# Kernel optimization log

Measured on AMD Instinct MI355X. Metric: run time of the kernel, lower is better.

The kernel has to match this reference:

```python
import jax, jax.numpy as jnp
import numpy as np

B, T, C, H, DH = 4, 2048, 1024, 16, 64  # batch, seq (block_size), n_embd, heads, head_size


def setup_inputs() -> dict:
    key = jax.random.key(0)
    ks = jax.random.split(key, 6)
    x = jax.random.normal(ks[0], (B, T, C), dtype=jnp.float32)
    init = 0.02
    Wq = jax.random.normal(ks[1], (H, C, DH), dtype=jnp.float32) * init
    Wk = jax.random.normal(ks[2], (H, C, DH), dtype=jnp.float32) * init
    Wv = jax.random.normal(ks[3], (H, C, DH), dtype=jnp.float32) * init
    Wp = jax.random.normal(ks[4], (H * DH, C), dtype=jnp.float32) * init
    bp = jnp.zeros((C,), dtype=jnp.float32)
    return {"x": x, "Wq": Wq, "Wk": Wk, "Wv": Wv, "Wp": Wp, "bp": bp}


def reference(x, Wq, Wk, Wv, Wp, bp):
    Bb, Tt, Cc = x.shape
    # per-head projections, vectorized over heads (original loops in Python)
    q = jnp.einsum('btc,hcd->bhtd', x, Wq)
    k = jnp.einsum('btc,hcd->bhtd', x, Wk)
    v = jnp.einsum('btc,hcd->bhtd', x, Wv)
    # NOTE: original scales by rsqrt(C) where C is the INPUT embed dim, not head_size
    scale = 1.0 / jnp.sqrt(jnp.asarray(Cc, dtype=x.dtype))
    wei = jnp.einsum('bhtd,bhsd->bhts', q, k) * scale  # [B,H,T,T]
    causal = jnp.tril(jnp.ones((Tt, Tt), dtype=bool))
    wei = jnp.where(causal, wei, -jnp.inf)
    wei = jax.nn.softmax(wei, axis=-1)
    out = jnp.einsum('bhts,bhsd->bhtd', wei, v)  # [B,H,T,DH]
    # concat heads along feature axis (head h -> slice h*DH:(h+1)*DH)
    out = out.transpose(0, 2, 1, 3).reshape(Bb, Tt, -1)  # [B,T,H*DH]
    out = out @ Wp + bp  # output projection to n_embd
    return out
```

## Files before the change

kernel.cpp:

```cpp
#include <hip/hip_runtime.h>

#define TSEQ 2048
#define CDIM 1024
#define NH 16
#define DH 64
#define NB 4

typedef __bf16 bf16x8 __attribute__((ext_vector_type(8)));
typedef float f32x4 __attribute__((ext_vector_type(4)));

#define QSCALE 0.04508422f

static __device__ __forceinline__ ushort f2bf(float f) {
  unsigned u = __float_as_uint(f);
  unsigned r = u + 0x7fffu + ((u >> 16) & 1u);
  return (ushort)(r >> 16);
}

static __device__ __forceinline__ void gload_lds16(const void* g, void* ldsbase) {
  __builtin_amdgcn_global_load_lds((const __attribute__((address_space(1))) void*)g,
                                   (__attribute__((address_space(3))) void*)ldsbase,
                                   16, 0, 0);
}

__global__ void cvt_x_kernel(const float4* __restrict__ src, ushort4* __restrict__ dst, int n4) {
  int i = blockIdx.x * blockDim.x + threadIdx.x;
  if (i >= n4) return;
  float4 f = src[i];
  ushort4 o;
  o.x = f2bf(f.x); o.y = f2bf(f.y); o.z = f2bf(f.z); o.w = f2bf(f.w);
  dst[i] = o;
}

__global__ void transpose_cvt_kernel(const float* __restrict__ src, ushort* __restrict__ dst,
                                     int R, int Cc) {
  __shared__ float tile[32][33];
  const float* s = src + (size_t)blockIdx.z * R * Cc;
  ushort* d = dst + (size_t)blockIdx.z * R * Cc;
  int c0 = blockIdx.x * 32, r0 = blockIdx.y * 32;
  int tx = threadIdx.x, ty = threadIdx.y;
  for (int i = ty; i < 32; i += 8) {
    int r = r0 + i, c = c0 + tx;
    tile[i][tx] = (r < R && c < Cc) ? s[(size_t)r * Cc + c] : 0.f;
  }
  __syncthreads();
  for (int i = ty; i < 32; i += 8) {
    int c = c0 + i, r = r0 + tx;
    if (c < Cc && r < R) d[(size_t)c * R + r] = f2bf(tile[tx][i]);
  }
}

__global__ __launch_bounds__(256) void qkv_kernel(
    const ushort* __restrict__ xb, const ushort* __restrict__ wqT,
    const ushort* __restrict__ wkT, const ushort* __restrict__ wvT,
    ushort* __restrict__ qb, ushort* __restrict__ kb, ushort* __restrict__ vTb) {
  __shared__ ushort lds[12288];
  const int tt = blockIdx.x, bh = blockIdx.y, sel = blockIdx.z;
  const int h = bh & (NH - 1);
  const int tid = threadIdx.x, w = tid >> 6, l = tid & 63;
  const ushort* A = xb + ((size_t)(bh >> 4) * TSEQ + (size_t)tt * 128) * CDIM;
  const ushort* Bw = (sel == 0 ? wqT : sel == 1 ? wkT : wvT) + (size_t)h * DH * CDIM;
  const int srow = l >> 3;
  const int scol = (((l & 7) ^ srow) << 3);
  char* ldsb = (char*)lds;

  f32x4 acc[2][4] = {};

  for (int k0 = 0; k0 < CDIM; k0 += 64) {
#pragma unroll
    for (int i = 0; i < 6; ++i) {
      int ch = w * 6 + i;
      if (ch < 16) {
        int row = ch * 8 + srow;
        gload_lds16(A + (size_t)row * CDIM + k0 + scol, ldsb + ch * 1024);
      } else {
        int row = (ch - 16) * 8 + srow;
        gload_lds16(Bw + (size_t)row * CDIM + k0 + scol, ldsb + 16384 + (ch - 16) * 1024);
      }
    }
    __syncthreads();
#pragma unroll
    for (int ks = 0; ks < 2; ++ks) {
      bf16x8 af[2];
#pragma unroll
      for (int fm = 0; fm < 2; ++fm) {
        int row = w * 32 + fm * 16 + (l & 15);
        int cb = (ks * 64 + 16 * (l >> 4)) ^ ((row & 7) << 4);
        af[fm] = *(const bf16x8*)(ldsb + row * 128 + cb);
      }
#pragma unroll
      for (int fn = 0; fn < 4; ++fn) {
        int n = fn * 16 + (l & 15);
        int cb = (ks * 64 + 16 * (l >> 4)) ^ ((n & 7) << 4);
        bf16x8 bfr = *(const bf16x8*)(ldsb + 16384 + n * 128 + cb);
#pragma unroll
        for (int fm = 0; fm < 2; ++fm)
          acc[fm][fn] = __builtin_amdgcn_mfma_f32_16x16x32_bf16(af[fm], bfr, acc[fm][fn], 0, 0, 0);
      }
    }
    __syncthreads();
  }

  const int tbase0 = tt * 128 + w * 32;
#pragma unroll
  for (int fm = 0; fm < 2; ++fm) {
#pragma unroll
    for (int fn = 0; fn < 4; ++fn) {
      int d = fn * 16 + (l & 15);
      int tb = tbase0 + fm * 16 + (l >> 4) * 4;
      if (sel == 2) {
        ushort4 pk;
        pk.x = f2bf(acc[fm][fn][0]); pk.y = f2bf(acc[fm][fn][1]);
        pk.z = f2bf(acc[fm][fn][2]); pk.w = f2bf(acc[fm][fn][3]);
        *(ushort4*)(vTb + ((size_t)bh * DH + d) * TSEQ + tb) = pk;
      } else if (sel == 0) {
#pragma unroll
        for (int r = 0; r < 4; ++r)
          qb[((size_t)bh * TSEQ + tb + r) * DH + d] = f2bf(acc[fm][fn][r] * QSCALE);
      } else {
#pragma unroll
        for (int r = 0; r < 4; ++r)
          kb[((size_t)bh * TSEQ + tb + r) * DH + d] = f2bf(acc[fm][fn][r]);
      }
    }
  }
}

__global__ __launch_bounds__(256) void attn_kernel(
    const ushort* __restrict__ qb, const ushort* __restrict__ kb,
    const ushort* __restrict__ vTb, ushort* __restrict__ aob) {
  __shared__ ushort lds[20992];
  char* ldsb = (char*)lds;
  const int tid = threadIdx.x, w = tid >> 6, l = tid & 63;
  const int id = blockIdx.x;
  const int bh = (id & 7) * 8 + ((id >> 3) & 7);
  const int pr = id >> 6;
  const int b = bh >> 4, h = bh & 15;
  const int g = l >> 4, q = l & 15;
  const int srow = l >> 3;
  const int scol = (((l & 7) ^ srow) << 3);
  char* pw = ldsb + 32768 + w * 2304;

#pragma unroll 1
  for (int pass = 0; pass < 2; ++pass) {
    const int qt = pass ? (31 - pr) : pr;
    const int q0 = qt * 64;
    const int nt = qt + 1;

    bf16x8 qf[2];
    {
      const ushort* qrow = qb + ((size_t)bh * TSEQ + q0 + w * 16 + q) * DH;
      qf[0] = *(const bf16x8*)(qrow + 8 * g);
      qf[1] = *(const bf16x8*)(qrow + 32 + 8 * g);
    }

    float m = -1e30f, lsum = 0.f;
    f32x4 o[4] = {};

#pragma unroll
    for (int i = 0; i < 4; ++i) {
      int ch = w * 4 + i;
      if (ch < 8)
        gload_lds16(kb + ((size_t)bh * TSEQ + ch * 8 + srow) * DH + scol, ldsb + ch * 1024);
      else {
        int d = (ch - 8) * 8 + srow;
        gload_lds16(vTb + ((size_t)bh * DH + d) * TSEQ + scol, ldsb + 16384 + (ch - 8) * 1024);
      }
    }

#pragma unroll 1
    for (int j = 0; j < nt; ++j) {
      __syncthreads();
      const int cbuf = j & 1;
      if (j + 1 < nt) {
        const int kv0 = (j + 1) * 64, nb = (j + 1) & 1;
#pragma unroll
        for (int i = 0; i < 4; ++i) {
          int ch = w * 4 + i;
          if (ch < 8)
            gload_lds16(kb + ((size_t)bh * TSEQ + kv0 + ch * 8 + srow) * DH + scol,
                        ldsb + nb * 8192 + ch * 1024);
          else {
            int d = (ch - 8) * 8 + srow;
            gload_lds16(vTb + ((size_t)bh * DH + d) * TSEQ + kv0 + scol,
                        ldsb + 16384 + nb * 8192 + (ch - 8) * 1024);
          }
        }
      }
      char* Kb = ldsb + cbuf * 8192;
      char* Vb = ldsb + 16384 + cbuf * 8192;

      f32x4 s[4] = {};
#pragma unroll
      for (int ks = 0; ks < 2; ++ks)
#pragma unroll
        for (int fn = 0; fn < 4; ++fn) {
          int n = fn * 16 + q;
          int cbb = (ks * 64 + 16 * g) ^ ((n & 7) << 4);
          bf16x8 kf = *(const bf16x8*)(Kb + n * 128 + cbb);
          s[fn] = __builtin_amdgcn_mfma_f32_16x16x32_bf16(kf, qf[ks], s[fn], 0, 0, 0);
        }

      if (j == nt - 1) {
#pragma unroll
        for (int fn = 0; fn < 4; ++fn)
#pragma unroll
          for (int r = 0; r < 4; ++r)
            if (fn * 16 + 4 * g + r > w * 16 + q) s[fn][r] = -1e30f;
      }

      float rm = fmaxf(fmaxf(s[0][0], s[0][1]), fmaxf(s[0][2], s[0][3]));
#pragma unroll
      for (int fn = 1; fn < 4; ++fn)
        rm = fmaxf(rm, fmaxf(fmaxf(s[fn][0], s[fn][1]), fmaxf(s[fn][2], s[fn][3])));
      rm = fmaxf(rm, __shfl_xor(rm, 16));
      rm = fmaxf(rm, __shfl_xor(rm, 32));

      if (__any(rm - m > 8.f)) {
        float mn = fmaxf(m, rm);
        float fc = __builtin_amdgcn_exp2f(m - mn);
        m = mn; lsum *= fc;
#pragma unroll
        for (int r = 0; r < 4; ++r) {
          float fcq = __shfl(fc, (l & 0x30) | (4 * g + r), 64);
#pragma unroll
          for (int fn = 0; fn < 4; ++fn) o[fn][r] *= fcq;
        }
      }

      float rs = 0.f;
#pragma unroll
      for (int fn = 0; fn < 4; ++fn) {
        float p0 = __builtin_amdgcn_exp2f(s[fn][0] - m);
        float p1 = __builtin_amdgcn_exp2f(s[fn][1] - m);
        float p2 = __builtin_amdgcn_exp2f(s[fn][2] - m);
        float p3 = __builtin_amdgcn_exp2f(s[fn][3] - m);
        rs += (p0 + p1) + (p2 + p3);
        uint u0 = (__float_as_uint(p0) >> 16) | (__float_as_uint(p1) & 0xffff0000u);
        uint u1 = (__float_as_uint(p2) >> 16) | (__float_as_uint(p3) & 0xffff0000u);
        *(uint2*)(pw + q * 144 + fn * 32 + g * 8) = make_uint2(u0, u1);
      }
      rs += __shfl_xor(rs, 16);
      rs += __shfl_xor(rs, 32);
      lsum += rs;

#pragma unroll
      for (int ks = 0; ks < 2; ++ks) {
        bf16x8 pf = *(const bf16x8*)(pw + q * 144 + ks * 64 + 16 * g);
#pragma unroll
        for (int fn = 0; fn < 4; ++fn) {
          int n = fn * 16 + q;
          int cbb = (ks * 64 + 16 * g) ^ ((n & 7) << 4);
          bf16x8 vf = *(const bf16x8*)(Vb + n * 128 + cbb);
          o[fn] = __builtin_amdgcn_mfma_f32_16x16x32_bf16(pf, vf, o[fn], 0, 0, 0);
        }
      }
    }

    float inv = 1.f / lsum;
#pragma unroll
    for (int r = 0; r < 4; ++r) {
      float invq = __shfl(inv, (l & 0x30) | (4 * g + r), 64);
      int t = q0 + w * 16 + 4 * g + r;
#pragma unroll
      for (int fn = 0; fn < 4; ++fn) {
        int d = fn * 16 + q;
        aob[((size_t)b * TSEQ + t) * (NH * DH) + h * DH + d] = f2bf(o[fn][r] * invq);
      }
    }
    __syncthreads();
  }
}

__global__ __launch_bounds__(256) void proj_kernel(
    const ushort* __restrict__ aob, const ushort* __restrict__ wpT,
    const float* __restrict__ bp, float* __restrict__ out) {
  __shared__ ushort lds[12288];
  const int mt = blockIdx.x, nt = blockIdx.y;
  const int tid = threadIdx.x, w = tid >> 6, l = tid & 63;
  const ushort* A = aob + (size_t)mt * 128 * CDIM;
  const ushort* Bw = wpT + (size_t)nt * 64 * CDIM;
  const int srow = l >> 3;
  const int scol = (((l & 7) ^ srow) << 3);
  char* ldsb = (char*)lds;
  f32x4 acc[2][4] = {};

  for (int k0 = 0; k0 < CDIM; k0 += 64) {
#pragma unroll
    for (int i = 0; i < 6; ++i) {
      int ch = w * 6 + i;
      if (ch < 16) {
        int row = ch * 8 + srow;
        gload_lds16(A + (size_t)row * CDIM + k0 + scol, ldsb + ch * 1024);
      } else {
        int row = (ch - 16) * 8 + srow;
        gload_lds16(Bw + (size_t)row * CDIM + k0 + scol, ldsb + 16384 + (ch - 16) * 1024);
      }
    }
    __syncthreads();
#pragma unroll
    for (int ks = 0; ks < 2; ++ks) {
      bf16x8 af[2];
#pragma unroll
      for (int fm = 0; fm < 2; ++fm) {
        int row = w * 32 + fm * 16 + (l & 15);
        int cb = (ks * 64 + 16 * (l >> 4)) ^ ((row & 7) << 4);
        af[fm] = *(const bf16x8*)(ldsb + row * 128 + cb);
      }
#pragma unroll
      for (int fn = 0; fn < 4; ++fn) {
        int n = fn * 16 + (l & 15);
        int cb = (ks * 64 + 16 * (l >> 4)) ^ ((n & 7) << 4);
        bf16x8 bfr = *(const bf16x8*)(ldsb + 16384 + n * 128 + cb);
#pragma unroll
        for (int fm = 0; fm < 2; ++fm)
          acc[fm][fn] = __builtin_amdgcn_mfma_f32_16x16x32_bf16(af[fm], bfr, acc[fm][fn], 0, 0, 0);
      }
    }
    __syncthreads();
  }

#pragma unroll
  for (int fm = 0; fm < 2; ++fm)
#pragma unroll
    for (int fn = 0; fn < 4; ++fn) {
      int colg = nt * 64 + fn * 16 + (l & 15);
      float bias = bp[colg];
#pragma unroll
      for (int r = 0; r < 4; ++r) {
        int row = mt * 128 + w * 32 + fm * 16 + (l >> 4) * 4 + r;
        out[(size_t)row * CDIM + colg] = acc[fm][fn][r] + bias;
      }
    }
}

extern "C" void kernel_launch(void* const* d_in, const int* in_sizes, int n_in,
                              void* d_out, int out_size, void* d_ws, size_t ws_size,
                              hipStream_t stream) {
  (void)in_sizes; (void)n_in; (void)out_size; (void)ws_size;
  const float* x  = (const float*)d_in[0];
  const float* Wq = (const float*)d_in[1];
  const float* Wk = (const float*)d_in[2];
  const float* Wv = (const float*)d_in[3];
  const float* Wp = (const float*)d_in[4];
  const float* bp = (const float*)d_in[5];
  float* out = (float*)d_out;
  char* ws = (char*)d_ws;

  ushort* xb  = (ushort*)(ws);
  ushort* wqT = (ushort*)(ws + (16ull << 20));
  ushort* wkT = (ushort*)(ws + (18ull << 20));
  ushort* wvT = (ushort*)(ws + (20ull << 20));
  ushort* wpT = (ushort*)(ws + (22ull << 20));
  ushort* qb  = (ushort*)(ws + (24ull << 20));
  ushort* kb  = (ushort*)(ws + (40ull << 20));
  ushort* vTb = (ushort*)(ws + (56ull << 20));
  ushort* aob = (ushort*)(ws + (72ull << 20));

  cvt_x_kernel<<<(NB * TSEQ * CDIM / 4 + 255) / 256, 256, 0, stream>>>(
      (const float4*)x, (ushort4*)xb, NB * TSEQ * CDIM / 4);
  transpose_cvt_kernel<<<dim3(2, 32, 16), dim3(32, 8), 0, stream>>>(Wq, wqT, CDIM, DH);
  transpose_cvt_kernel<<<dim3(2, 32, 16), dim3(32, 8), 0, stream>>>(Wk, wkT, CDIM, DH);
  transpose_cvt_kernel<<<dim3(2, 32, 16), dim3(32, 8), 0, stream>>>(Wv, wvT, CDIM, DH);
  transpose_cvt_kernel<<<dim3(32, 32, 1), dim3(32, 8), 0, stream>>>(Wp, wpT, CDIM, CDIM);

  qkv_kernel<<<dim3(16, 64, 3), 256, 0, stream>>>(xb, wqT, wkT, wvT, qb, kb, vTb);
  attn_kernel<<<dim3(1024), 256, 0, stream>>>(qb, kb, vTb, aob);
  proj_kernel<<<dim3(64, 16), 256, 0, stream>>>(aob, wpT, bp, out);
}
```

Measured before the change: 202.2 us.

## Unify QKV/proj GEMMs into 128x128-tile kernel and keep P in registers

Replaces the separate QKV and projection GEMMs with one templated kernel that uses 128x128 output tiles, a 2x2 warp layout and an XCD-aware block remap, raising data reuse per tile. The Q/K/V weights are treated as one concatenated N=3072 matrix. In attention, the softmax probabilities are packed with v_cvt_pk_bf16_f32 and redistributed through ds_bpermute instead of a round trip through LDS. This shrinks LDS use and adds a launch bound for higher occupancy. The costs are more accumulator registers in the GEMMs and extra permute instructions in attention.

```diff
diff --git a/kernel.cpp b/kernel.cpp
--- a/kernel.cpp
+++ b/kernel.cpp
@@ -15,6 +15,12 @@
   unsigned u = __float_as_uint(f);
   unsigned r = u + 0x7fffu + ((u >> 16) & 1u);
   return (ushort)(r >> 16);
+}
+
+static __device__ __forceinline__ uint cvtpk(float lo, float hi) {
+  uint r;
+  asm("v_cvt_pk_bf16_f32 %0, %1, %2" : "=v"(r) : "v"(lo), "v"(hi));
+  return r;
 }
 
 static __device__ __forceinline__ void gload_lds16(const void* g, void* ldsbase) {
@@ -50,86 +56,95 @@
   }
 }
 
-__global__ __launch_bounds__(256) void qkv_kernel(
-    const ushort* __restrict__ xb, const ushort* __restrict__ wqT,
-    const ushort* __restrict__ wkT, const ushort* __restrict__ wvT,
+template <int MODE>
+__global__ __launch_bounds__(256) void gemm_kernel(
+    const ushort* __restrict__ A, const ushort* __restrict__ Bt,
+    const float* __restrict__ bp, float* __restrict__ fout,
     ushort* __restrict__ qb, ushort* __restrict__ kb, ushort* __restrict__ vTb) {
-  __shared__ ushort lds[12288];
-  const int tt = blockIdx.x, bh = blockIdx.y, sel = blockIdx.z;
-  const int h = bh & (NH - 1);
+  __shared__ ushort lds[16384];
   const int tid = threadIdx.x, w = tid >> 6, l = tid & 63;
-  const ushort* A = xb + ((size_t)(bh >> 4) * TSEQ + (size_t)tt * 128) * CDIM;
-  const ushort* Bw = (sel == 0 ? wqT : sel == 1 ? wkT : wvT) + (size_t)h * DH * CDIM;
+  const int nwg = gridDim.x;
+  const int bid = blockIdx.x;
+  const int wgid = (bid & 7) * (nwg >> 3) + (bid >> 3);
+  const int mt = wgid & 63, nt = wgid >> 6;
+  const int wr = w >> 1, wc = w & 1;
   const int srow = l >> 3;
   const int scol = (((l & 7) ^ srow) << 3);
   char* ldsb = (char*)lds;
 
-  f32x4 acc[2][4] = {};
+  f32x4 acc[4][4] = {};
 
   for (int k0 = 0; k0 < CDIM; k0 += 64) {
 #pragma unroll
-    for (int i = 0; i < 6; ++i) {
-      int ch = w * 6 + i;
+    for (int i = 0; i < 8; ++i) {
+      int ch = w * 8 + i;
       if (ch < 16) {
-        int row = ch * 8 + srow;
-        gload_lds16(A + (size_t)row * CDIM + k0 + scol, ldsb + ch * 1024);
+        gload_lds16(A + ((size_t)mt * 128 + ch * 8 + srow) * CDIM + k0 + scol, ldsb + ch * 1024);
       } else {
-        int row = (ch - 16) * 8 + srow;
-        gload_lds16(Bw + (size_t)row * CDIM + k0 + scol, ldsb + 16384 + (ch - 16) * 1024);
+        gload_lds16(Bt + ((size_t)nt * 128 + (ch - 16) * 8 + srow) * CDIM + k0 + scol,
+                    ldsb + ch * 1024);
       }
     }
     __syncthreads();
 #pragma unroll
     for (int ks = 0; ks < 2; ++ks) {
-      bf16x8 af[2];
-#pragma unroll
-      for (int fm = 0; fm < 2; ++fm) {
-        int row = w * 32 + fm * 16 + (l & 15);
+      bf16x8 af[4];
+#pragma unroll
+      for (int fm = 0; fm < 4; ++fm) {
+        int row = wr * 64 + fm * 16 + (l & 15);
         int cb = (ks * 64 + 16 * (l >> 4)) ^ ((row & 7) << 4);
         af[fm] = *(const bf16x8*)(ldsb + row * 128 + cb);
       }
 #pragma unroll
       for (int fn = 0; fn < 4; ++fn) {
-        int n = fn * 16 + (l & 15);
+        int n = wc * 64 + fn * 16 + (l & 15);
         int cb = (ks * 64 + 16 * (l >> 4)) ^ ((n & 7) << 4);
         bf16x8 bfr = *(const bf16x8*)(ldsb + 16384 + n * 128 + cb);
 #pragma unroll
-        for (int fm = 0; fm < 2; ++fm)
+        for (int fm = 0; fm < 4; ++fm)
           acc[fm][fn] = __builtin_amdgcn_mfma_f32_16x16x32_bf16(af[fm], bfr, acc[fm][fn], 0, 0, 0);
       }
     }
     __syncthreads();
   }
 
-  const int tbase0 = tt * 128 + w * 32;
-#pragma unroll
-  for (int fm = 0; fm < 2; ++fm) {
+#pragma unroll
+  for (int fm = 0; fm < 4; ++fm) {
 #pragma unroll
     for (int fn = 0; fn < 4; ++fn) {
-      int d = fn * 16 + (l & 15);
-      int tb = tbase0 + fm * 16 + (l >> 4) * 4;
-      if (sel == 2) {
-        ushort4 pk;
-        pk.x = f2bf(acc[fm][fn][0]); pk.y = f2bf(acc[fm][fn][1]);
-        pk.z = f2bf(acc[fm][fn][2]); pk.w = f2bf(acc[fm][fn][3]);
-        *(ushort4*)(vTb + ((size_t)bh * DH + d) * TSEQ + tb) = pk;
-      } else if (sel == 0) {
+      const int gr0 = mt * 128 + wr * 64 + fm * 16 + (l >> 4) * 4;
+      const int gc = nt * 128 + wc * 64 + fn * 16 + (l & 15);
+      if (MODE == 1) {
+        float bias = bp[gc];
 #pragma unroll
         for (int r = 0; r < 4; ++r)
-          qb[((size_t)bh * TSEQ + tb + r) * DH + d] = f2bf(acc[fm][fn][r] * QSCALE);
+          fout[(size_t)(gr0 + r) * CDIM + gc] = acc[fm][fn][r] + bias;
       } else {
-#pragma unroll
-        for (int r = 0; r < 4; ++r)
-          kb[((size_t)bh * TSEQ + tb + r) * DH + d] = f2bf(acc[fm][fn][r]);
-      }
-    }
-  }
-}
-
-__global__ __launch_bounds__(256) void attn_kernel(
+        const int sel = gc >> 10, h = (gc >> 6) & 15, d = gc & 63;
+        const int bh = (gr0 >> 11) * NH + h, tl = gr0 & 2047;
+        if (sel == 2) {
+          ushort4 pk;
+          pk.x = f2bf(acc[fm][fn][0]); pk.y = f2bf(acc[fm][fn][1]);
+          pk.z = f2bf(acc[fm][fn][2]); pk.w = f2bf(acc[fm][fn][3]);
+          *(ushort4*)(vTb + ((size_t)bh * DH + d) * TSEQ + tl) = pk;
+        } else if (sel == 0) {
+#pragma unroll
+          for (int r = 0; r < 4; ++r)
+            qb[((size_t)bh * TSEQ + tl + r) * DH + d] = f2bf(acc[fm][fn][r] * QSCALE);
+        } else {
+#pragma unroll
+          for (int r = 0; r < 4; ++r)
+            kb[((size_t)bh * TSEQ + tl + r) * DH + d] = f2bf(acc[fm][fn][r]);
+        }
+      }
+    }
+  }
+}
+
+__global__ __launch_bounds__(256, 4) void attn_kernel(
     const ushort* __restrict__ qb, const ushort* __restrict__ kb,
     const ushort* __restrict__ vTb, ushort* __restrict__ aob) {
-  __shared__ ushort lds[20992];
+  __shared__ ushort lds[16384];
   char* ldsb = (char*)lds;
   const int tid = threadIdx.x, w = tid >> 6, l = tid & 63;
   const int id = blockIdx.x;
@@ -139,7 +154,9 @@
   const int g = l >> 4, q = l & 15;
   const int srow = l >> 3;
   const int scol = (((l & 7) ^ srow) << 3);
-  char* pw = ldsb + 32768 + w * 2304;
+  const int adrA = ((l & 16) << 1 | q) << 2;
+  const int adrB = adrA + 64;
+  const bool hi32 = (l & 32) != 0;
 
 #pragma unroll 1
   for (int pass = 0; pass < 2; ++pass) {
@@ -209,10 +226,10 @@
             if (fn * 16 + 4 * g + r > w * 16 + q) s[fn][r] = -1e30f;
       }
 
-      float rm = fmaxf(fmaxf(s[0][0], s[0][1]), fmaxf(s[0][2], s[0][3]));
-#pragma unroll
-      for (int fn = 1; fn < 4; ++fn)
-        rm = fmaxf(rm, fmaxf(fmaxf(s[fn][0], s[fn][1]), fmaxf(s[fn][2], s[fn][3])));
+      float rm = fmaxf(fmaxf(fmaxf(s[0][0], s[0][1]), fmaxf(s[0][2], s[0][3])),
+                       fmaxf(fmaxf(s[1][0], s[1][1]), fmaxf(s[1][2], s[1][3])));
+      rm = fmaxf(rm, fmaxf(fmaxf(fmaxf(s[2][0], s[2][1]), fmaxf(s[2][2], s[2][3])),
+                           fmaxf(fmaxf(s[3][0], s[3][1]), fmaxf(s[3][2], s[3][3]))));
       rm = fmaxf(rm, __shfl_xor(rm, 16));
       rm = fmaxf(rm, __shfl_xor(rm, 32));
 
@@ -228,6 +245,7 @@
         }
       }
 
+      uint D[4][2];
       float rs = 0.f;
 #pragma unroll
       for (int fn = 0; fn < 4; ++fn) {
@@ -236,9 +254,8 @@
         float p2 = __builtin_amdgcn_exp2f(s[fn][2] - m);
         float p3 = __builtin_amdgcn_exp2f(s[fn][3] - m);
         rs += (p0 + p1) + (p2 + p3);
-        uint u0 = (__float_as_uint(p0) >> 16) | (__float_as_uint(p1) & 0xffff0000u);
-        uint u1 = (__float_as_uint(p2) >> 16) | (__float_as_uint(p3) & 0xffff0000u);
-        *(uint2*)(pw + q * 144 + fn * 32 + g * 8) = make_uint2(u0, u1);
+        D[fn][0] = cvtpk(p0, p1);
+        D[fn][1] = cvtpk(p2, p3);
       }
       rs += __shfl_xor(rs, 16);
       rs += __shfl_xor(rs, 32);
@@ -246,13 +263,25 @@
 
 #pragma unroll
       for (int ks = 0; ks < 2; ++ks) {
-        bf16x8 pf = *(const bf16x8*)(pw + q * 144 + ks * 64 + 16 * g);
+        uint t0a = __builtin_amdgcn_ds_bpermute(adrA, (int)D[2 * ks][0]);
+        uint t0b = __builtin_amdgcn_ds_bpermute(adrA, (int)D[2 * ks + 1][0]);
+        uint t1a = __builtin_amdgcn_ds_bpermute(adrA, (int)D[2 * ks][1]);
+        uint t1b = __builtin_amdgcn_ds_bpermute(adrA, (int)D[2 * ks + 1][1]);
+        uint t2a = __builtin_amdgcn_ds_bpermute(adrB, (int)D[2 * ks][0]);
+        uint t2b = __builtin_amdgcn_ds_bpermute(adrB, (int)D[2 * ks + 1][0]);
+        uint t3a = __builtin_amdgcn_ds_bpermute(adrB, (int)D[2 * ks][1]);
+        uint t3b = __builtin_amdgcn_ds_bpermute(adrB, (int)D[2 * ks + 1][1]);
+        union { uint u[4]; bf16x8 v; } P;
+        P.u[0] = hi32 ? t0b : t0a;
+        P.u[1] = hi32 ? t1b : t1a;
+        P.u[2] = hi32 ? t2b : t2a;
+        P.u[3] = hi32 ? t3b : t3a;
 #pragma unroll
         for (int fn = 0; fn < 4; ++fn) {
           int n = fn * 16 + q;
           int cbb = (ks * 64 + 16 * g) ^ ((n & 7) << 4);
           bf16x8 vf = *(const bf16x8*)(Vb + n * 128 + cbb);
-          o[fn] = __builtin_amdgcn_mfma_f32_16x16x32_bf16(pf, vf, o[fn], 0, 0, 0);
+          o[fn] = __builtin_amdgcn_mfma_f32_16x16x32_bf16(P.v, vf, o[fn], 0, 0, 0);
         }
       }
     }
@@ -270,68 +299,6 @@
     }
     __syncthreads();
   }
-}
-
-__global__ __launch_bounds__(256) void proj_kernel(
-    const ushort* __restrict__ aob, const ushort* __restrict__ wpT,
-    const float* __restrict__ bp, float* __restrict__ out) {
-  __shared__ ushort lds[12288];
-  const int mt = blockIdx.x, nt = blockIdx.y;
-  const int tid = threadIdx.x, w = tid >> 6, l = tid & 63;
-  const ushort* A = aob + (size_t)mt * 128 * CDIM;
-  const ushort* Bw = wpT + (size_t)nt * 64 * CDIM;
-  const int srow = l >> 3;
-  const int scol = (((l & 7) ^ srow) << 3);
-  char* ldsb = (char*)lds;
-  f32x4 acc[2][4] = {};
-
-  for (int k0 = 0; k0 < CDIM; k0 += 64) {
-#pragma unroll
-    for (int i = 0; i < 6; ++i) {
-      int ch = w * 6 + i;
-      if (ch < 16) {
-        int row = ch * 8 + srow;
-        gload_lds16(A + (size_t)row * CDIM + k0 + scol, ldsb + ch * 1024);
-      } else {
-        int row = (ch - 16) * 8 + srow;
-        gload_lds16(Bw + (size_t)row * CDIM + k0 + scol, ldsb + 16384 + (ch - 16) * 1024);
-      }
-    }
-    __syncthreads();
-#pragma unroll
-    for (int ks = 0; ks < 2; ++ks) {
-      bf16x8 af[2];
-#pragma unroll
-      for (int fm = 0; fm < 2; ++fm) {
-        int row = w * 32 + fm * 16 + (l & 15);
-        int cb = (ks * 64 + 16 * (l >> 4)) ^ ((row & 7) << 4);
-        af[fm] = *(const bf16x8*)(ldsb + row * 128 + cb);
-      }
-#pragma unroll
-      for (int fn = 0; fn < 4; ++fn) {
-        int n = fn * 16 + (l & 15);
-        int cb = (ks * 64 + 16 * (l >> 4)) ^ ((n & 7) << 4);
-        bf16x8 bfr = *(const bf16x8*)(ldsb + 16384 + n * 128 + cb);
-#pragma unroll
-        for (int fm = 0; fm < 2; ++fm)
-          acc[fm][fn] = __builtin_amdgcn_mfma_f32_16x16x32_bf16(af[fm], bfr, acc[fm][fn], 0, 0, 0);
-      }
-    }
-    __syncthreads();
-  }
-
-#pragma unroll
-  for (int fm = 0; fm < 2; ++fm)
-#pragma unroll
-    for (int fn = 0; fn < 4; ++fn) {
-      int colg = nt * 64 + fn * 16 + (l & 15);
-      float bias = bp[colg];
-#pragma unroll
-      for (int r = 0; r < 4; ++r) {
-        int row = mt * 128 + w * 32 + fm * 16 + (l >> 4) * 4 + r;
-        out[(size_t)row * CDIM + colg] = acc[fm][fn][r] + bias;
-      }
-    }
 }
 
 extern "C" void kernel_launch(void* const* d_in, const int* in_sizes, int n_in,
@@ -348,9 +315,10 @@
   char* ws = (char*)d_ws;
 
   ushort* xb  = (ushort*)(ws);
-  ushort* wqT = (ushort*)(ws + (16ull << 20));
-  ushort* wkT = (ushort*)(ws + (18ull << 20));
-  ushort* wvT = (ushort*)(ws + (20ull << 20));
+  ushort* wall = (ushort*)(ws + (16ull << 20));
+  ushort* wqT = wall;
+  ushort* wkT = wall + (1ull << 20);
+  ushort* wvT = wall + (2ull << 20);
   ushort* wpT = (ushort*)(ws + (22ull << 20));
   ushort* qb  = (ushort*)(ws + (24ull << 20));
   ushort* kb  = (ushort*)(ws + (40ull << 20));
@@ -364,7 +332,7 @@
   transpose_cvt_kernel<<<dim3(2, 32, 16), dim3(32, 8), 0, stream>>>(Wv, wvT, CDIM, DH);
   transpose_cvt_kernel<<<dim3(32, 32, 1), dim3(32, 8), 0, stream>>>(Wp, wpT, CDIM, CDIM);
 
-  qkv_kernel<<<dim3(16, 64, 3), 256, 0, stream>>>(xb, wqT, wkT, wvT, qb, kb, vTb);
+  gemm_kernel<0><<<dim3(64 * 24), 256, 0, stream>>>(xb, wall, nullptr, nullptr, qb, kb, vTb);
   attn_kernel<<<dim3(1024), 256, 0, stream>>>(qb, kb, vTb, aob);
-  proj_kernel<<<dim3(64, 16), 256, 0, stream>>>(aob, wpT, bp, out);
-}
+  gemm_kernel<1><<<dim3(64 * 8), 256, 0, stream>>>(aob, wpT, bp, out, nullptr, nullptr, nullptr);
+}
```

New measurement: 203.8 us. No clear change (+0.8%).
